# Performance work log

Measured on AMD Instinct MI355X. Metric: run time of the kernel, lower is better.

Reference implementation:

```python
import jax, jax.numpy as jnp
import numpy as np

N = 8192       # batch size
BIT = 32       # hash code length
NCLASS = 100   # number of classes
ALPHA = 0.1    # config['alpha'] (quantization weight)
BEITA = 1.0    # config['beita'] (classification weight)
GAMMA = 0.1    # config['gamma'] (balancing weight)
P = 2          # config['p']


def setup_inputs() -> dict:
    key = jax.random.key(0)
    k1, k2, k3 = jax.random.split(key, 3)
    u = jax.random.normal(k1, (N, BIT), dtype=jnp.float32)
    Y = jax.random.normal(k2, (N, NCLASS), dtype=jnp.float32)
    labels = jax.random.randint(k3, (N,), 0, NCLASS)
    y = jax.nn.one_hot(labels, NCLASS, dtype=jnp.float32)  # one-hot targets
    return {"u": u, "Y": Y, "y": y}


def _hash_loss(u, y):
    n = u.shape[0]
    theta = (u @ u.T) * 0.5                       # [N, N]
    sim = (y @ y.T > 0).astype(u.dtype)           # [N, N] pairwise same-class
    # log(1 + exp(theta)) - Sim * theta  (logaddexp = stable same math)
    pair = jnp.logaddexp(0.0, theta) - sim * theta
    mask_pos = sim > 0
    s1 = sim.sum() - n                            # positives minus diagonal
    s0 = n * n - sim.sum()                        # negatives
    s0 = jnp.where(s0 == 0, 1.0, s0)
    s1 = jnp.where(s1 == 0, 1.0, s1)
    s = s0 + s1
    scale = jnp.where(mask_pos, s / s1, s / s0)
    pair = pair * scale
    # original subtracts diag of the *detached* rescaled matrix
    pair = pair - jax.lax.stop_gradient(jnp.diag(jnp.diag(pair)))
    count = n * (n - 1) / 2
    return pair.sum() / 2.0 / count


def reference(u, Y, y):
    likelihood_loss = _hash_loss(u, y)
    # CrossEntropyLoss with soft (one-hot float) targets
    logp = jax.nn.log_softmax(Y, axis=-1)
    classification_loss = -(y * logp).sum(axis=-1).mean()
    m = u.mean(axis=1)
    if P == 1:
        quantization_loss = ALPHA * jnp.abs(m).mean()
    else:
        quantization_loss = ALPHA * (m ** 2).mean()
    b = jnp.sign(u)
    balancing_loss = GAMMA * ((u - b) ** 2).mean()
    return likelihood_loss + BEITA * classification_loss + quantization_loss + balancing_loss
```

## Files before the change

kernel.cpp:

```cpp
#include <hip/hip_runtime.h>
#include <math.h>

#define N 8192
#define BIT 32
#define NCLASS 100
#define ALPHA 0.1
#define BEITA 1.0
#define GAMMA 0.1

#define BT 128
#define NT (N / BT)
#define NPAIRBLK (NT * (NT + 1) / 2)
#define NPREP (N / 8)

#define SCALE_BF 0.84932181f
#define LN2 0.6931471805599453

typedef __attribute__((ext_vector_type(8))) short s16x8;
typedef __attribute__((ext_vector_type(4))) float f32x4;

#if __has_builtin(__builtin_amdgcn_exp2f)
static __device__ __forceinline__ float fexp2(float x) { return __builtin_amdgcn_exp2f(x); }
#else
static __device__ __forceinline__ float fexp2(float x) { return exp2f(x); }
#endif
#if __has_builtin(__builtin_amdgcn_logf)
static __device__ __forceinline__ float flog2(float x) { return __builtin_amdgcn_logf(x); }
#else
static __device__ __forceinline__ float flog2(float x) { return __log2f(x); }
#endif

static __device__ __forceinline__ unsigned short f2bf(float f) {
    unsigned int x = __float_as_uint(f);
    x += 0x7fff + ((x >> 16) & 1);
    return (unsigned short)(x >> 16);
}


__global__ __launch_bounds__(256) void prep_kernel(
    const float* __restrict__ u, const float* __restrict__ Y, const float* __restrict__ y,
    unsigned char* __restrict__ lab8, unsigned short* __restrict__ ubf,
    double* __restrict__ Pc, double* __restrict__ Pm, double* __restrict__ Pb)
{
    const int t = threadIdx.x;
    const int lane = t & 63;
    const int w = t >> 6;
    const int row0 = blockIdx.x * 8;

    float wcls = 0.f;
    #pragma unroll
    for (int rr = 0; rr < 2; ++rr) {
        const int r = row0 + w * 2 + rr;
        const float* Yp = Y + (size_t)r * NCLASS;
        const float* yp = y + (size_t)r * NCLASS;
        const bool has2 = lane < (NCLASS - 64);
        float Y0 = Yp[lane];
        float Y1 = has2 ? Yp[64 + lane] : -1e30f;
        float y0 = yp[lane];
        float y1 = has2 ? yp[64 + lane] : 0.f;
        float m = fmaxf(Y0, Y1);
        #pragma unroll
        for (int o = 32; o; o >>= 1) m = fmaxf(m, __shfl_xor(m, o, 64));
        float e  = __expf(Y0 - m) + (has2 ? __expf(Y1 - m) : 0.f);
        float tg = y0 * Y0 + (has2 ? y1 * Y1 : 0.f);
        #pragma unroll
        for (int o = 32; o; o >>= 1) { e += __shfl_xor(e, o, 64); tg += __shfl_xor(tg, o, 64); }
        unsigned long long b0 = __ballot(y0 > 0.5f);
        unsigned long long b1 = __ballot(has2 && (y1 > 0.5f));
        if (lane == 0) {
            int lbl = b0 ? (__ffsll((long long)b0) - 1) : (64 + __ffsll((long long)b1) - 1);
            lab8[r] = (unsigned char)lbl;
            wcls += m + __logf(e) - tg;
        }
    }

    const size_t uidx = (size_t)row0 * BIT + t;
    const float x = u[uidx];
    ubf[uidx] = f2bf(x * SCALE_BF);
    float bb = (x > 0.f) ? 1.f : ((x < 0.f) ? -1.f : 0.f);
    float d = x - bb;
    float bal = d * d;
    float rs = x;
    #pragma unroll
    for (int o = 1; o < 32; o <<= 1) rs += __shfl_xor(rs, o, 64);
    float mrow = rs * (1.f / BIT);
    float m2 = ((t & 31) == 0) ? mrow * mrow : 0.f;
    #pragma unroll
    for (int o = 32; o; o >>= 1) { m2 += __shfl_down(m2, o, 64); bal += __shfl_down(bal, o, 64); }

    __shared__ double red[4][3];
    if (lane == 0) { red[w][0] = (double)wcls; red[w][1] = (double)m2; red[w][2] = (double)bal; }
    __syncthreads();
    if (t == 0) {
        Pc[blockIdx.x] = red[0][0] + red[1][0] + red[2][0] + red[3][0];
        Pm[blockIdx.x] = red[0][1] + red[1][1] + red[2][1] + red[3][1];
        Pb[blockIdx.x] = red[0][2] + red[1][2] + red[2][2] + red[3][2];
    }
}

__global__ __launch_bounds__(256, 4) void pair_kernel(
    const unsigned short* __restrict__ ubf, const unsigned char* __restrict__ lab8,
    double* __restrict__ Ppos, double* __restrict__ Pneg)
{
    const int b = blockIdx.x;
    int ti = (int)(((float)(2 * NT + 1) - sqrtf((float)((2 * NT + 1) * (2 * NT + 1) - 8 * b))) * 0.5f);
    int S = ti * (2 * NT - ti + 1) / 2;
    if (S > b) { --ti; S = ti * (2 * NT - ti + 1) / 2; }
    else { int S2 = (ti + 1) * (2 * NT - ti) / 2; if (S2 <= b) { ++ti; S = S2; } }
    const int tj = ti + (b - S);
    const int i0 = ti * BT, j0 = tj * BT;
    const bool offd = (ti != tj);

    const int t = threadIdx.x;
    const int lane = t & 63;
    const int w = t >> 6;
    const int wy = w >> 1, wx = w & 1;
    const int quad = lane >> 4, lr = lane & 15;
    const int ar = i0 + wy * 64;
    const int br = j0 + wx * 64;

    s16x8 av[4], bv[4];
    #pragma unroll
    for (int x = 0; x < 4; ++x) {
        av[x] = *(const s16x8*)(ubf + (size_t)(ar + x * 16 + lr) * BIT + quad * 8);
        bv[x] = *(const s16x8*)(ubf + (size_t)(br + x * 16 + lr) * BIT + quad * 8);
    }
    int lavp[4], lbv[4];
    #pragma unroll
    for (int a = 0; a < 4; ++a) lavp[a] = *(const int*)(lab8 + ar + a * 16 + quad * 4);
    #pragma unroll
    for (int c = 0; c < 4; ++c) lbv[c] = (int)lab8[br + c * 16 + lr];

    f32x4 acc[4][4];
    #pragma unroll
    for (int a = 0; a < 4; ++a)
        #pragma unroll
        for (int c = 0; c < 4; ++c)
            acc[a][c] = __builtin_amdgcn_mfma_f32_16x16x32_bf16(
                av[a], bv[c], (f32x4){0.f, 0.f, 0.f, 0.f}, 0, 0, 0);

    float sp0 = 0.f, sp1 = 0.f, sn0 = 0.f, sn1 = 0.f;
    #pragma unroll
    for (int a = 0; a < 4; ++a) {
        #pragma unroll
        for (int r = 0; r < 4; ++r) {
            const int la = (lavp[a] >> (r * 8)) & 0xff;
            const int rowv = wy * 64 + a * 16 + quad * 4 + r;
            #pragma unroll
            for (int c = 0; c < 4; ++c) {
                const float tv = acc[a][c][r];
                float sl = flog2(1.f + fexp2(tv));
                float d  = sl - tv;
                const bool sim  = (la == lbv[c]);
                const bool keep = offd | ((wx * 64 + c * 16 + lr) > rowv);
                float up = (sim & keep)  ? d  : 0.f;
                float un = (keep & !sim) ? sl : 0.f;
                if (r & 1) { sp1 += up; sn1 += un; }
                else       { sp0 += up; sn0 += un; }
            }
        }
    }

    float sp = sp0 + sp1, sn = sn0 + sn1;
    #pragma unroll
    for (int o = 32; o; o >>= 1) { sp += __shfl_down(sp, o, 64); sn += __shfl_down(sn, o, 64); }
    __shared__ float wredp[4], wredn[4];
    if (lane == 0) { wredp[w] = sp; wredn[w] = sn; }
    __syncthreads();
    if (t == 0) {
        Ppos[b] = (double)wredp[0] + (double)wredp[1] + (double)wredp[2] + (double)wredp[3];
        Pneg[b] = (double)wredn[0] + (double)wredn[1] + (double)wredn[2] + (double)wredn[3];
    }
}

__global__ __launch_bounds__(256) void fin_kernel(
    const unsigned char* __restrict__ lab8, const double* __restrict__ Ppos,
    const double* __restrict__ Pneg, const double* __restrict__ Pc,
    const double* __restrict__ Pm, const double* __restrict__ Pb, float* __restrict__ out)
{
    __shared__ int h[128];
    __shared__ double red[4][5];
    __shared__ double scd[2];
    const int t = threadIdx.x;
    const int lane = t & 63;
    const int w = t >> 6;

    if (t < 128) h[t] = 0;
    __syncthreads();
    #pragma unroll
    for (int k = 0; k < 32; ++k) atomicAdd(&h[lab8[t + k * 256]], 1);
    __syncthreads();

    if (w == 0) {
        long long c0 = (lane < NCLASS) ? h[lane] : 0;
        long long c1 = (lane + 64 < NCLASS) ? h[lane + 64] : 0;
        long long ss = c0 * c0 + c1 * c1;
        #pragma unroll
        for (int o = 32; o; o >>= 1) ss += __shfl_xor(ss, o, 64);
        if (lane == 0) {
            double s1 = (double)ss - (double)N;
            double s0 = (double)N * (double)N - (double)ss;
            if (s0 == 0.0) s0 = 1.0;
            if (s1 == 0.0) s1 = 1.0;
            double s = s0 + s1;
            scd[0] = (s / s1) * LN2;
            scd[1] = (s / s0) * LN2;
        }
    }

    double p0 = 0, p1 = 0, cc = 0, mm = 0, bb = 0;
    for (int i = t; i < NPAIRBLK; i += 256) { p0 += Ppos[i]; p1 += Pneg[i]; }
    for (int i = t; i < NPREP; i += 256)    { cc += Pc[i]; mm += Pm[i]; bb += Pb[i]; }
    #pragma unroll
    for (int o = 32; o; o >>= 1) {
        p0 += __shfl_down(p0, o, 64); p1 += __shfl_down(p1, o, 64);
        cc += __shfl_down(cc, o, 64); mm += __shfl_down(mm, o, 64);
        bb += __shfl_down(bb, o, 64);
    }
    if (lane == 0) { red[w][0] = p0; red[w][1] = p1; red[w][2] = cc; red[w][3] = mm; red[w][4] = bb; }
    __syncthreads();
    if (t == 0) {
        double a_pos = red[0][0] + red[1][0] + red[2][0] + red[3][0];
        double a_neg = red[0][1] + red[1][1] + red[2][1] + red[3][1];
        double a_cls = red[0][2] + red[1][2] + red[2][2] + red[3][2];
        double a_m2  = red[0][3] + red[1][3] + red[2][3] + red[3][3];
        double a_bal = red[0][4] + red[1][4] + red[2][4] + red[3][4];
        double pairsum = scd[0] * a_pos + scd[1] * a_neg;
        double lik   = 2.0 * pairsum / ((double)N * (double)(N - 1));
        double cls   = a_cls / (double)N;
        double quant = ALPHA * (a_m2 / (double)N);
        double bal   = GAMMA * (a_bal / ((double)N * (double)BIT));
        out[0] = (float)(lik + BEITA * cls + quant + bal);
    }
}

extern "C" void kernel_launch(void* const* d_in, const int* in_sizes, int n_in,
                              void* d_out, int out_size, void* d_ws, size_t ws_size,
                              hipStream_t stream) {
    const float* u = (const float*)d_in[0];
    const float* Y = (const float*)d_in[1];
    const float* y = (const float*)d_in[2];
    float* out = (float*)d_out;

    char* ws = (char*)d_ws;
    unsigned char*  lab8 = (unsigned char*)(ws + 1024);
    unsigned short* ubf  = (unsigned short*)(ws + 16384);
    double* Ppos = (double*)(ws + 557056);
    double* Pneg = (double*)(ws + 581632);
    double* Pc   = (double*)(ws + 606208);
    double* Pm   = (double*)(ws + 614400);
    double* Pb   = (double*)(ws + 622592);

    prep_kernel<<<NPREP, 256, 0, stream>>>(u, Y, y, lab8, ubf, Pc, Pm, Pb);
    pair_kernel<<<NPAIRBLK, 256, 0, stream>>>(ubf, lab8, Ppos, Pneg);
    fin_kernel<<<1, 256, 0, stream>>>(lab8, Ppos, Pneg, Pc, Pm, Pb, out);
}
```

Measured before the change: 90.27 us.

## Specialize diagonal tiles, fold sim sign into softplus, write per-wave partials

The pair loop now computes one softplus per element, taking the argument as -theta for similar pairs and theta otherwise, instead of softplus followed by a subtraction. It separates the two cases by accumulating the total and the similar-only sum. A compile-time template splits diagonal tiles (which need the upper-triangle mask) from off-diagonal tiles, which skip the mask entirely. The shared-memory block reduction and __syncthreads are removed; each wave writes its own partial sums, which quadruples the partial array the final kernel must reduce and requires moving the workspace offsets.

```diff
diff --git a/kernel.cpp b/kernel.cpp
--- a/kernel.cpp
+++ b/kernel.cpp
@@ -1,5 +1,6 @@
 #include <hip/hip_runtime.h>
 #include <math.h>
+#include <type_traits>
 
 #define N 8192
 #define BIT 32
@@ -11,6 +12,7 @@
 #define BT 128
 #define NT (N / BT)
 #define NPAIRBLK (NT * (NT + 1) / 2)
+#define NPW (NPAIRBLK * 4)
 #define NPREP (N / 8)
 
 #define SCALE_BF 0.84932181f
@@ -109,7 +111,6 @@
     else { int S2 = (ti + 1) * (2 * NT - ti) / 2; if (S2 <= b) { ++ti; S = S2; } }
     const int tj = ti + (b - S);
     const int i0 = ti * BT, j0 = tj * BT;
-    const bool offd = (ti != tj);
 
     const int t = threadIdx.x;
     const int lane = t & 63;
@@ -139,37 +140,41 @@
             acc[a][c] = __builtin_amdgcn_mfma_f32_16x16x32_bf16(
                 av[a], bv[c], (f32x4){0.f, 0.f, 0.f, 0.f}, 0, 0, 0);
 
-    float sp0 = 0.f, sp1 = 0.f, sn0 = 0.f, sn1 = 0.f;
-    #pragma unroll
-    for (int a = 0; a < 4; ++a) {
-        #pragma unroll
-        for (int r = 0; r < 4; ++r) {
-            const int la = (lavp[a] >> (r * 8)) & 0xff;
-            const int rowv = wy * 64 + a * 16 + quad * 4 + r;
+    float vsum0 = 0.f, vsum1 = 0.f, vsim0 = 0.f, vsim1 = 0.f;
+    auto run = [&](auto DIAGC) {
+        constexpr bool DIAG = decltype(DIAGC)::value;
+        #pragma unroll
+        for (int a = 0; a < 4; ++a) {
             #pragma unroll
-            for (int c = 0; c < 4; ++c) {
-                const float tv = acc[a][c][r];
-                float sl = flog2(1.f + fexp2(tv));
-                float d  = sl - tv;
-                const bool sim  = (la == lbv[c]);
-                const bool keep = offd | ((wx * 64 + c * 16 + lr) > rowv);
-                float up = (sim & keep)  ? d  : 0.f;
-                float un = (keep & !sim) ? sl : 0.f;
-                if (r & 1) { sp1 += up; sn1 += un; }
-                else       { sp0 += up; sn0 += un; }
+            for (int r = 0; r < 4; ++r) {
+                const int la = (lavp[a] >> (r * 8)) & 0xff;
+                const int rowv = a * 16 + quad * 4 + r;
+                #pragma unroll
+                for (int c = 0; c < 4; ++c) {
+                    const float tv = acc[a][c][r];
+                    const bool sim = (la == lbv[c]);
+                    float x = sim ? -tv : tv;
+                    float v = flog2(1.f + fexp2(x));
+                    if (DIAG) {
+                        const bool keep = (c * 16 + lr) > rowv;
+                        v = keep ? v : 0.f;
+                    }
+                    float vs = sim ? v : 0.f;
+                    if (r & 1) { vsum1 += v; vsim1 += vs; }
+                    else       { vsum0 += v; vsim0 += vs; }
+                }
             }
         }
-    }
-
-    float sp = sp0 + sp1, sn = sn0 + sn1;
-    #pragma unroll
-    for (int o = 32; o; o >>= 1) { sp += __shfl_down(sp, o, 64); sn += __shfl_down(sn, o, 64); }
-    __shared__ float wredp[4], wredn[4];
-    if (lane == 0) { wredp[w] = sp; wredn[w] = sn; }
-    __syncthreads();
-    if (t == 0) {
-        Ppos[b] = (double)wredp[0] + (double)wredp[1] + (double)wredp[2] + (double)wredp[3];
-        Pneg[b] = (double)wredn[0] + (double)wredn[1] + (double)wredn[2] + (double)wredn[3];
+    };
+    if (ti == tj) run(std::integral_constant<bool, true>{});
+    else          run(std::integral_constant<bool, false>{});
+
+    float vsum = vsum0 + vsum1, vsim = vsim0 + vsim1;
+    #pragma unroll
+    for (int o = 32; o; o >>= 1) { vsum += __shfl_down(vsum, o, 64); vsim += __shfl_down(vsim, o, 64); }
+    if (lane == 0) {
+        Ppos[4 * b + w] = (double)vsim;
+        Pneg[4 * b + w] = (double)(vsum - vsim);
     }
 }
 
@@ -209,8 +214,8 @@
     }
 
     double p0 = 0, p1 = 0, cc = 0, mm = 0, bb = 0;
-    for (int i = t; i < NPAIRBLK; i += 256) { p0 += Ppos[i]; p1 += Pneg[i]; }
-    for (int i = t; i < NPREP; i += 256)    { cc += Pc[i]; mm += Pm[i]; bb += Pb[i]; }
+    for (int i = t; i < NPW; i += 256)   { p0 += Ppos[i]; p1 += Pneg[i]; }
+    for (int i = t; i < NPREP; i += 256) { cc += Pc[i]; mm += Pm[i]; bb += Pb[i]; }
     #pragma unroll
     for (int o = 32; o; o >>= 1) {
         p0 += __shfl_down(p0, o, 64); p1 += __shfl_down(p1, o, 64);
@@ -246,10 +251,10 @@
     unsigned char*  lab8 = (unsigned char*)(ws + 1024);
     unsigned short* ubf  = (unsigned short*)(ws + 16384);
     double* Ppos = (double*)(ws + 557056);
-    double* Pneg = (double*)(ws + 581632);
-    double* Pc   = (double*)(ws + 606208);
-    double* Pm   = (double*)(ws + 614400);
-    double* Pb   = (double*)(ws + 622592);
+    double* Pneg = (double*)(ws + 630784);
+    double* Pc   = (double*)(ws + 704512);
+    double* Pm   = (double*)(ws + 712704);
+    double* Pb   = (double*)(ws + 720896);
 
     prep_kernel<<<NPREP, 256, 0, stream>>>(u, Y, y, lab8, ubf, Pc, Pm, Pb);
     pair_kernel<<<NPAIRBLK, 256, 0, stream>>>(ubf, lab8, Ppos, Pneg);
```

Measured after the change: 93.83 us. +3.9%, slower.
